# Optimization experiments

Measured on AMD Instinct MI355X. Metric: run time of the kernel, lower is better.

Reference implementation:

```python
import jax, jax.numpy as jnp
import numpy as np
import math

PI = math.pi


def setup_inputs() -> dict:
    key = jax.random.key(0)
    k1, k2 = jax.random.split(key)
    x = jax.random.normal(k1, (8, 512, 512, 16), dtype=jnp.float32)
    w_angle = jax.random.normal(k2, (16, 1), dtype=jnp.float32) * 0.1
    b_angle = jnp.zeros((1,), dtype=jnp.float32)
    return {"x": x, "w_angle": w_angle, "b_angle": b_angle}


def _rotate_one(img, ang):
    # img: [H, W, C]; ang: scalar angle (radians, CCW), matching tfa.image.rotate
    H, W, C = img.shape
    dt = img.dtype
    c = jnp.cos(ang)
    s = jnp.sin(ang)
    # tfa angles_to_projective_transforms: rotate about image center
    x_off = ((W - 1) - (c * (W - 1) - s * (H - 1))) / 2.0
    y_off = ((H - 1) - (s * (W - 1) + c * (H - 1))) / 2.0
    oy, ox = jnp.meshgrid(jnp.arange(H, dtype=dt), jnp.arange(W, dtype=dt), indexing="ij")
    # inverse affine: output pixel -> input coordinate
    ix = c * ox - s * oy + x_off
    iy = s * ox + c * oy + y_off
    x0 = jnp.floor(ix)
    y0 = jnp.floor(iy)
    wx = (ix - x0)[..., None]
    wy = (iy - y0)[..., None]

    def read(yy, xx):
        # CONSTANT fill mode: out-of-bounds reads are 0
        valid = (xx >= 0) & (xx <= W - 1) & (yy >= 0) & (yy <= H - 1)
        xi = jnp.clip(xx, 0, W - 1).astype(jnp.int32)
        yi = jnp.clip(yy, 0, H - 1).astype(jnp.int32)
        return img[yi, xi] * valid[..., None].astype(dt)

    top = read(y0, x0) * (1.0 - wx) + read(y0, x0 + 1.0) * wx
    bot = read(y0 + 1.0, x0) * (1.0 - wx) + read(y0 + 1.0, x0 + 1.0) * wx
    return top * (1.0 - wy) + bot * wy


def reference(x, w_angle, b_angle):
    # x: [B, H, W, C]
    mean_features = jnp.mean(x, axis=(1, 2))                    # [B, C]
    angle_normed = jnp.tanh(mean_features @ w_angle + b_angle)  # [B, 1]
    pi = jnp.asarray(PI, dtype=x.dtype)
    angle = jnp.clip(angle_normed[:, 0] * pi, -pi, pi)          # [B]
    return jax.vmap(_rotate_one)(x, angle)
```

## Files before the change

### kernel.cpp

```cpp
#include <hip/hip_runtime.h>
#include <math.h>

#define HW     512
#define CH     16
#define PIXELS (HW * HW)
#define BATCH  8
#define RED_SLICES 128

__global__ __launch_bounds__(256) void reduce_partial_kernel(
        const float* __restrict__ x, float* __restrict__ partial) {
    const int b = blockIdx.x >> 7;
    const int s = blockIdx.x & (RED_SLICES - 1);
    const float4* xp = (const float4*)(x + (size_t)b * PIXELS * CH);
    int idx = s * 8192 + threadIdx.x;
    float4 acc = make_float4(0.f, 0.f, 0.f, 0.f);
#pragma unroll 8
    for (int k = 0; k < 32; ++k) {
        float4 v = xp[idx + k * 256];
        acc.x += v.x; acc.y += v.y; acc.z += v.z; acc.w += v.w;
    }
    for (int off = 4; off < 64; off <<= 1) {
        acc.x += __shfl_xor(acc.x, off);
        acc.y += __shfl_xor(acc.y, off);
        acc.z += __shfl_xor(acc.z, off);
        acc.w += __shfl_xor(acc.w, off);
    }
    __shared__ float swave[4][CH];
    const int wave = threadIdx.x >> 6;
    const int lane = threadIdx.x & 63;
    if (lane < 4) {
        swave[wave][lane * 4 + 0] = acc.x;
        swave[wave][lane * 4 + 1] = acc.y;
        swave[wave][lane * 4 + 2] = acc.z;
        swave[wave][lane * 4 + 3] = acc.w;
    }
    __syncthreads();
    if (threadIdx.x < CH) {
        float t = swave[0][threadIdx.x] + swave[1][threadIdx.x]
                + swave[2][threadIdx.x] + swave[3][threadIdx.x];
        partial[(size_t)blockIdx.x * CH + threadIdx.x] = t;
    }
}

__global__ void angle_kernel(const float* __restrict__ partial,
                             const float* __restrict__ w_angle,
                             const float* __restrict__ b_angle,
                             float* __restrict__ params) {
    __shared__ float mean_s[BATCH][CH];
    const int t = threadIdx.x;
    if (t < BATCH * CH) {
        const int b = t >> 4;
        const int c = t & 15;
        float sum = 0.f;
        for (int s = 0; s < RED_SLICES; ++s)
            sum += partial[(size_t)(b * RED_SLICES + s) * CH + c];
        mean_s[b][c] = sum * (1.0f / (float)PIXELS);
    }
    __syncthreads();
    if (t < BATCH) {
        float dot = 0.f;
        for (int c = 0; c < CH; ++c) dot += mean_s[t][c] * w_angle[c];
        float tn = tanhf(dot + b_angle[0]);
        const float pi = 3.14159265358979323846f;
        float ang = fminf(fmaxf(tn * pi, -pi), pi);
        float cs = cosf(ang);
        float sn = sinf(ang);
        float x_off = (511.0f - (cs * 511.0f - sn * 511.0f)) * 0.5f;
        float y_off = (511.0f - (sn * 511.0f + cs * 511.0f)) * 0.5f;
        params[t * 4 + 0] = cs;
        params[t * 4 + 1] = sn;
        params[t * 4 + 2] = x_off;
        params[t * 4 + 3] = y_off;
    }
}

__global__ __launch_bounds__(256) void rotate_kernel(
        const float* __restrict__ x, const float* __restrict__ params,
        float* __restrict__ out) {
    const int g = blockIdx.x * 256 + threadIdx.x;
    const int q   = g & 3;
    const int pix = g >> 2;
    const int b   = pix >> 18;
    const int p   = pix & (PIXELS - 1);
    const int oy  = p >> 9;
    const int ox  = p & (HW - 1);

    const float cs = params[b * 4 + 0];
    const float sn = params[b * 4 + 1];
    const float xo = params[b * 4 + 2];
    const float yo = params[b * 4 + 3];

    const float fx = (float)ox;
    const float fy = (float)oy;
    const float ix = cs * fx - sn * fy + xo;
    const float iy = sn * fx + cs * fy + yo;
    const float x0f = floorf(ix);
    const float y0f = floorf(iy);
    const float wx = ix - x0f;
    const float wy = iy - y0f;
    const int x0 = (int)x0f;
    const int y0 = (int)y0f;

    const float4* base = (const float4*)x + ((size_t)b * PIXELS) * 4 + q;
    auto read = [&](int yy, int xx) -> float4 {
        if ((unsigned)xx < (unsigned)HW && (unsigned)yy < (unsigned)HW)
            return base[((size_t)yy * HW + xx) * 4];
        return make_float4(0.f, 0.f, 0.f, 0.f);
    };

    float4 v00 = read(y0,     x0);
    float4 v01 = read(y0,     x0 + 1);
    float4 v10 = read(y0 + 1, x0);
    float4 v11 = read(y0 + 1, x0 + 1);

    const float wx1 = 1.0f - wx;
    const float wy1 = 1.0f - wy;
    float4 r;
    r.x = (v00.x * wx1 + v01.x * wx) * wy1 + (v10.x * wx1 + v11.x * wx) * wy;
    r.y = (v00.y * wx1 + v01.y * wx) * wy1 + (v10.y * wx1 + v11.y * wx) * wy;
    r.z = (v00.z * wx1 + v01.z * wx) * wy1 + (v10.z * wx1 + v11.z * wx) * wy;
    r.w = (v00.w * wx1 + v01.w * wx) * wy1 + (v10.w * wx1 + v11.w * wx) * wy;

    ((float4*)out)[g] = r;
}

extern "C" void kernel_launch(void* const* d_in, const int* in_sizes, int n_in,
                              void* d_out, int out_size, void* d_ws, size_t ws_size,
                              hipStream_t stream) {
    const float* x       = (const float*)d_in[0];
    const float* w_angle = (const float*)d_in[1];
    const float* b_angle = (const float*)d_in[2];
    float* out = (float*)d_out;

    float* partial = (float*)d_ws;
    float* params  = partial + BATCH * RED_SLICES * CH;

    reduce_partial_kernel<<<BATCH * RED_SLICES, 256, 0, stream>>>(x, partial);
    angle_kernel<<<1, 128, 0, stream>>>(partial, w_angle, b_angle, params);
    rotate_kernel<<<BATCH * PIXELS * 4 / 256, 256, 0, stream>>>(x, params, out);
}
```

Before: 72.01 us.

## Swizzle rotate block order, fast-path interior reads, nontemporal stores, double-precision angle

The block index in the rotate kernel is remapped so that consecutive blocks come from different batch images. This spreads the work across XCDs and their L2 caches. The rotate kernel also gains a branch-light fast path for interior pixels, and its output is written with nontemporal stores so the write-only result does not pollute cache. Separately, the angle computation is moved to double precision for accuracy, which has negligible cost in a single tiny block. The swizzle could hurt locality if the hardware's block dispatch does not line up with it.

```diff
diff --git a/kernel.cpp b/kernel.cpp
--- a/kernel.cpp
+++ b/kernel.cpp
@@ -6,6 +6,8 @@
 #define PIXELS (HW * HW)
 #define BATCH  8
 #define RED_SLICES 128
+
+typedef float f32x4 __attribute__((ext_vector_type(4)));
 
 __global__ __launch_bounds__(256) void reduce_partial_kernel(
         const float* __restrict__ x, float* __restrict__ partial) {
@@ -46,38 +48,40 @@
                              const float* __restrict__ w_angle,
                              const float* __restrict__ b_angle,
                              float* __restrict__ params) {
-    __shared__ float mean_s[BATCH][CH];
+    __shared__ double mean_s[BATCH][CH];
     const int t = threadIdx.x;
     if (t < BATCH * CH) {
         const int b = t >> 4;
         const int c = t & 15;
-        float sum = 0.f;
+        double sum = 0.0;
         for (int s = 0; s < RED_SLICES; ++s)
-            sum += partial[(size_t)(b * RED_SLICES + s) * CH + c];
-        mean_s[b][c] = sum * (1.0f / (float)PIXELS);
+            sum += (double)partial[(size_t)(b * RED_SLICES + s) * CH + c];
+        mean_s[b][c] = sum * (1.0 / (double)PIXELS);
     }
     __syncthreads();
     if (t < BATCH) {
-        float dot = 0.f;
-        for (int c = 0; c < CH; ++c) dot += mean_s[t][c] * w_angle[c];
-        float tn = tanhf(dot + b_angle[0]);
-        const float pi = 3.14159265358979323846f;
-        float ang = fminf(fmaxf(tn * pi, -pi), pi);
-        float cs = cosf(ang);
-        float sn = sinf(ang);
-        float x_off = (511.0f - (cs * 511.0f - sn * 511.0f)) * 0.5f;
-        float y_off = (511.0f - (sn * 511.0f + cs * 511.0f)) * 0.5f;
-        params[t * 4 + 0] = cs;
-        params[t * 4 + 1] = sn;
-        params[t * 4 + 2] = x_off;
-        params[t * 4 + 3] = y_off;
+        double dot = 0.0;
+        for (int c = 0; c < CH; ++c) dot += mean_s[t][c] * (double)w_angle[c];
+        double tn = tanh(dot + (double)b_angle[0]);
+        const double pi = 3.14159265358979323846;
+        double ang = fmin(fmax(tn * pi, -pi), pi);
+        double cs = cos(ang);
+        double sn = sin(ang);
+        double x_off = (511.0 - (cs * 511.0 - sn * 511.0)) * 0.5;
+        double y_off = (511.0 - (sn * 511.0 + cs * 511.0)) * 0.5;
+        params[t * 4 + 0] = (float)cs;
+        params[t * 4 + 1] = (float)sn;
+        params[t * 4 + 2] = (float)x_off;
+        params[t * 4 + 3] = (float)y_off;
     }
 }
 
 __global__ __launch_bounds__(256) void rotate_kernel(
         const float* __restrict__ x, const float* __restrict__ params,
         float* __restrict__ out) {
-    const int g = blockIdx.x * 256 + threadIdx.x;
+    int bid = blockIdx.x;
+    bid = ((bid & 7) << 12) | (bid >> 3);
+    const int g = bid * 256 + threadIdx.x;
     const int q   = g & 3;
     const int pix = g >> 2;
     const int b   = pix >> 18;
@@ -102,26 +106,36 @@
     const int y0 = (int)y0f;
 
     const float4* base = (const float4*)x + ((size_t)b * PIXELS) * 4 + q;
-    auto read = [&](int yy, int xx) -> float4 {
-        if ((unsigned)xx < (unsigned)HW && (unsigned)yy < (unsigned)HW)
-            return base[((size_t)yy * HW + xx) * 4];
-        return make_float4(0.f, 0.f, 0.f, 0.f);
-    };
 
-    float4 v00 = read(y0,     x0);
-    float4 v01 = read(y0,     x0 + 1);
-    float4 v10 = read(y0 + 1, x0);
-    float4 v11 = read(y0 + 1, x0 + 1);
+    float4 v00, v01, v10, v11;
+    if (x0 >= 0 && y0 >= 0 && x0 < HW - 1 && y0 < HW - 1) {
+        const float4* row0 = base + (size_t)y0 * (HW * 4);
+        v00 = row0[(size_t)x0 * 4];
+        v01 = row0[(size_t)(x0 + 1) * 4];
+        const float4* row1 = row0 + HW * 4;
+        v10 = row1[(size_t)x0 * 4];
+        v11 = row1[(size_t)(x0 + 1) * 4];
+    } else {
+        auto read = [&](int yy, int xx) -> float4 {
+            if ((unsigned)xx < (unsigned)HW && (unsigned)yy < (unsigned)HW)
+                return base[((size_t)yy * HW + xx) * 4];
+            return make_float4(0.f, 0.f, 0.f, 0.f);
+        };
+        v00 = read(y0,     x0);
+        v01 = read(y0,     x0 + 1);
+        v10 = read(y0 + 1, x0);
+        v11 = read(y0 + 1, x0 + 1);
+    }
 
     const float wx1 = 1.0f - wx;
     const float wy1 = 1.0f - wy;
-    float4 r;
+    f32x4 r;
     r.x = (v00.x * wx1 + v01.x * wx) * wy1 + (v10.x * wx1 + v11.x * wx) * wy;
     r.y = (v00.y * wx1 + v01.y * wx) * wy1 + (v10.y * wx1 + v11.y * wx) * wy;
     r.z = (v00.z * wx1 + v01.z * wx) * wy1 + (v10.z * wx1 + v11.z * wx) * wy;
     r.w = (v00.w * wx1 + v01.w * wx) * wy1 + (v10.w * wx1 + v11.w * wx) * wy;
 
-    ((float4*)out)[g] = r;
+    __builtin_nontemporal_store(r, (f32x4*)out + g);
 }
 
 extern "C" void kernel_launch(void* const* d_in, const int* in_sizes, int n_in,
```

Result: faster. 67.90 us (-5.7%).
